# Kernel tuning notes

Measured on AMD Instinct MI355X. Metric: run time of the kernel, lower is better.

Reference implementation:

```python
import jax, jax.numpy as jnp
import numpy as np

L = 2000          # number of residues (sequence length)
FEATURES_L = 2048 # config.features_L pad target
W = 7             # config.window_size
D = 54            # per-residue feature dim after bert_lin
H = 3             # attention heads
HD = D // H       # head dim = 18
CH = 32           # conv hidden channels
KS = (3, 5, 7)    # config.kernels


def setup_inputs() -> dict:
    key = jax.random.key(0)
    ks = jax.random.split(key, 20)
    n = lambda k, s, sc=0.02: jax.random.normal(k, s, jnp.float32) * sc
    return {
        'beft_f': jax.random.normal(ks[0], (L, 1024), jnp.float32),
        'pssm_f': jax.random.normal(ks[1], (L, 20), jnp.float32),
        'hmm_f': jax.random.normal(ks[2], (L, 30), jnp.float32),
        'dssp_f': jax.random.normal(ks[3], (L, 14), jnp.float32),
        'W_bert': n(ks[4], (1024, D)), 'b_bert': jnp.zeros((D,), jnp.float32),
        'ln_g1': jnp.ones((D,), jnp.float32), 'ln_b1': jnp.zeros((D,), jnp.float32),
        'ln_g2': jnp.ones((D,), jnp.float32), 'ln_b2': jnp.zeros((D,), jnp.float32),
        'conv1_w': n(ks[5], (CH, 1, 3, 1), 0.1), 'conv1_b': n(ks[6], (CH,), 0.1),
        'prelu_a': jnp.array(0.25, jnp.float32),
        'conv2_w': n(ks[7], (CH, 1, 5, 1), 0.1), 'conv2_b': n(ks[8], (CH,), 0.1),
        'conv3_w': n(ks[9], (CH, 1, 7, 1), 0.1), 'conv3_b': n(ks[10], (CH,), 0.1),
        'W1': n(ks[11], (972, 256)), 'b1': jnp.zeros((256,), jnp.float32),
        'W2': n(ks[12], (CH * 256, 256)), 'b2': jnp.zeros((256,), jnp.float32),
    }


def _ln(x, g, b, eps=1e-5):
    m = x.mean(-1, keepdims=True)
    v = ((x - m) ** 2).mean(-1, keepdims=True)
    return (x - m) * jax.lax.rsqrt(v + eps) * g + b


def _attn(x, g, b):
    # x: (L, W, D); no qkv projections, no 1/sqrt(d) scaling (as in source)
    qh = x.reshape(x.shape[0], W, H, HD)
    s = jnp.einsum('bqhd,bkhd->bhqk', qh, qh)
    p = jax.nn.softmax(s, axis=-1)
    o = jnp.einsum('bhqk,bkhd->bqhd', p, qh).reshape(x.shape[0], W, D)
    return _ln(o, g, b)


def _conv_branch(x, w, bias, k, act):
    pad = (k - 1) // 2
    c = jax.lax.conv_general_dilated(x, w, (1, 1), ((pad, pad), (0, 0)),
                                     dimension_numbers=('NCHW', 'OIHW', 'NCHW'))
    c = act(c + bias[None, :, None, None])
    c = jax.lax.reduce_window(c, -jnp.inf, jax.lax.max,
                              (1, 1, k, 1), (1, 1, 1, 1), 'VALID')
    return c.reshape(c.shape[0], CH, -1)  # (FEATURES_L, 32, (W-k+1)*2D)


def _forward(beft_f, W_bert, b_bert, ln_g1, ln_b1, ln_g2, ln_b2,
             conv1_w, conv1_b, prelu_a, conv2_w, conv2_b, conv3_w, conv3_b,
             W1, b1, W2, b2):
    f = beft_f @ W_bert + b_bert  # (L, 54)
    # sliding-window gather replicating the source python loop exactly:
    # interior rows i in (W, L-W): window = f[i-4 : i+3]; boundary rows: [f[i], 0...0]
    i = jnp.arange(L)
    j = jnp.arange(W)
    gidx = jnp.clip(i[:, None] - (W // 2 + 1) + j[None, :], 0, L - 1)
    win_int = f[gidx]                                   # (L, 7, 54)
    win_bnd = jnp.zeros((L, W, D), f.dtype).at[:, 0].set(f)
    boundary = (i <= W) | (i + W >= L)
    new_f = jnp.where(boundary[:, None, None], win_bnd, win_int)
    sf = _attn(new_f, ln_g1, ln_b1)
    sf = _attn(sf, ln_g2, ln_b2)
    cat = jnp.concatenate([new_f, sf], axis=2)          # (L, 7, 108)
    x = jnp.pad(cat, ((0, FEATURES_L - L), (0, 0), (0, 0)))[:, None]  # (FL,1,7,108)
    prelu = lambda z: jnp.where(z >= 0, z, prelu_a * z)
    feats = jnp.concatenate([
        _conv_branch(x, conv1_w, conv1_b, KS[0], prelu),
        _conv_branch(x, conv2_w, conv2_b, KS[1], jax.nn.relu),
        _conv_branch(x, conv3_w, conv3_b, KS[2], jax.nn.relu)], axis=2)  # (FL,32,972)
    y = feats[:L] @ W1 + b1                             # (L, 32, 256)
    y = y.reshape(L, CH * 256) @ W2 + b2                # (L, 256)
    return jnp.where(y >= 0, y, 0.01 * y)               # leaky_relu


def reference(beft_f, pssm_f, hmm_f, dssp_f, W_bert, b_bert, ln_g1, ln_b1,
              ln_g2, ln_b2, conv1_w, conv1_b, prelu_a, conv2_w, conv2_b,
              conv3_w, conv3_b, W1, b1, W2, b2):
    # pssm_f / hmm_f / dssp_f are accepted but unused in the source forward
    return _forward(beft_f, W_bert, b_bert, ln_g1, ln_b1, ln_g2, ln_b2,
                    conv1_w, conv1_b, prelu_a, conv2_w, conv2_b,
                    conv3_w, conv3_b, W1, b1, W2, b2)
```

## Files before the change

kernel.cpp:

```cpp
#include <hip/hip_runtime.h>

#define L_RES 2000
#define DF 54
#define WIN 7

typedef short bf16x8 __attribute__((ext_vector_type(8)));
typedef float f32x4 __attribute__((ext_vector_type(4)));
typedef unsigned short ushort8v __attribute__((ext_vector_type(8)));

__device__ __forceinline__ unsigned short f2bf(float f) {
    unsigned int u = __float_as_uint(f);
    unsigned int r = (u + 0x7FFFu + ((u >> 16) & 1u)) >> 16;
    return (unsigned short)r;
}
__device__ __forceinline__ float bf2f(unsigned short h) {
    return __uint_as_float(((unsigned int)h) << 16);
}
__device__ __forceinline__ void gload16(const unsigned short* g, unsigned short* l) {
    __builtin_amdgcn_global_load_lds(
        (const __attribute__((address_space(1))) void*)g,
        (__attribute__((address_space(3))) void*)l, 16, 0, 0);
}

__global__ __launch_bounds__(256) void split_beft(const float* __restrict__ beft,
                                                  unsigned short* __restrict__ A2) {
    int l = blockIdx.x;
    int t = threadIdx.x;
    unsigned short* row = A2 + (size_t)l * 3072;
    for (int k = t; k < 1024; k += 256) {
        unsigned short hi = 0, lo = 0;
        if (l < L_RES) {
            float x = beft[(size_t)l * 1024 + k];
            hi = f2bf(x);
            lo = f2bf(x - bf2f(hi));
        }
        row[k] = hi;
        row[1024 + k] = lo;
        row[2048 + k] = hi;
    }
}

__global__ __launch_bounds__(256) void b2t_build(const float* __restrict__ Wb,
                                                 unsigned short* __restrict__ B2T) {
    int idx = blockIdx.x * 256 + threadIdx.x;
    int n = idx / 3072, col = idx % 3072;
    int seg = col >> 10, k = col & 1023;
    unsigned short r = 0;
    if (n < DF) {
        float v = Wb[(size_t)k * DF + n];
        unsigned short hi = f2bf(v);
        r = (seg < 2) ? hi : f2bf(v - bf2f(hi));
    }
    B2T[idx] = r;
}

__global__ __launch_bounds__(256) void bert_mfma(const unsigned short* __restrict__ A2,
                                                 const unsigned short* __restrict__ B2T,
                                                 float* __restrict__ bpart) {
    __shared__ unsigned short ldsA[128 * 64];
    __shared__ unsigned short ldsB[64 * 64];
    int t = threadIdx.x, w = t >> 6, lane = t & 63;
    int m0 = blockIdx.x * 128;
    int z = blockIdx.y;
    long koff = (long)z * 768;
    int wr = w >> 1, wc = w & 1;
    int arow = lane & 15, kgrp = lane >> 4;

    const unsigned short* aS[4]; const unsigned short* bS[2];
    int aD[4], bD[2];
    #pragma unroll
    for (int j = 0; j < 4; ++j) {
        int s = j * 256 + t, r = s >> 3, c = s & 7;
        aS[j] = A2 + koff + (size_t)(m0 + r) * 3072 + c * 8;
        aD[j] = r * 64 + ((c ^ (r & 7)) * 8);
    }
    #pragma unroll
    for (int j = 0; j < 2; ++j) {
        int s = j * 256 + t, r = s >> 3, c = s & 7;
        bS[j] = B2T + koff + (size_t)r * 3072 + c * 8;
        bD[j] = r * 64 + ((c ^ (r & 7)) * 8);
    }
    f32x4 acc[4][2];
    #pragma unroll
    for (int mi = 0; mi < 4; ++mi)
        #pragma unroll
        for (int ni = 0; ni < 2; ++ni) acc[mi][ni] = (f32x4)(0.f);

    ushort8v va[4], vb[2];
    #pragma unroll
    for (int j = 0; j < 4; ++j) va[j] = *(const ushort8v*)(aS[j]);
    #pragma unroll
    for (int j = 0; j < 2; ++j) vb[j] = *(const ushort8v*)(bS[j]);

    for (int ks = 0; ks < 12; ++ks) {
        __syncthreads();
        #pragma unroll
        for (int j = 0; j < 4; ++j) *(ushort8v*)&ldsA[aD[j]] = va[j];
        #pragma unroll
        for (int j = 0; j < 2; ++j) *(ushort8v*)&ldsB[bD[j]] = vb[j];
        __syncthreads();
        if (ks + 1 < 12) {
            #pragma unroll
            for (int j = 0; j < 4; ++j) va[j] = *(const ushort8v*)(aS[j] + (ks + 1) * 64);
            #pragma unroll
            for (int j = 0; j < 2; ++j) vb[j] = *(const ushort8v*)(bS[j] + (ks + 1) * 64);
        }
        #pragma unroll
        for (int kk = 0; kk < 2; ++kk) {
            int chunk = kk * 4 + kgrp;
            bf16x8 af[4], bfr[2];
            #pragma unroll
            for (int mi = 0; mi < 4; ++mi) {
                int rl = wr * 64 + mi * 16 + arow;
                af[mi] = *(const bf16x8*)&ldsA[rl * 64 + ((chunk ^ (rl & 7)) * 8)];
            }
            #pragma unroll
            for (int ni = 0; ni < 2; ++ni) {
                int rl = wc * 32 + ni * 16 + arow;
                bfr[ni] = *(const bf16x8*)&ldsB[rl * 64 + ((chunk ^ (rl & 7)) * 8)];
            }
            #pragma unroll
            for (int mi = 0; mi < 4; ++mi)
                #pragma unroll
                for (int ni = 0; ni < 2; ++ni)
                    acc[mi][ni] = __builtin_amdgcn_mfma_f32_16x16x32_bf16(af[mi], bfr[ni], acc[mi][ni], 0, 0, 0);
        }
    }
    #pragma unroll
    for (int ni = 0; ni < 2; ++ni) {
        int n = wc * 32 + ni * 16 + arow;
        #pragma unroll
        for (int mi = 0; mi < 4; ++mi)
            #pragma unroll
            for (int r = 0; r < 4; ++r) {
                int m = m0 + wr * 64 + mi * 16 + kgrp * 4 + r;
                bpart[((size_t)z * 2048 + m) * 64 + n] = acc[mi][ni][r];
            }
    }
}

__global__ __launch_bounds__(64) void bert_reduce(const float* __restrict__ bpart,
                                                  const float* __restrict__ bb,
                                                  float* __restrict__ f) {
    int l = blockIdx.x, n = threadIdx.x;
    if (n < DF) {
        float s = bb[n];
        #pragma unroll
        for (int z = 0; z < 4; ++z) s += bpart[((size_t)z * 2048 + l) * 64 + n];
        f[(size_t)l * DF + n] = s;
    }
}

__device__ __forceinline__ void attn_layer_w(const float (*in)[DF], float (*out)[DF],
                                             float (*s)[WIN][WIN],
                                             const float* __restrict__ g,
                                             const float* __restrict__ b,
                                             float* mm, float* vv, int lane) {
    for (int idx = lane; idx < 3 * WIN * WIN; idx += 64) {
        int h = idx / 49, r = idx % 49, q = r / WIN, k = r % WIN;
        float sum = 0.f;
        #pragma unroll
        for (int d = 0; d < 18; ++d) sum = fmaf(in[q][h * 18 + d], in[k][h * 18 + d], sum);
        s[h][q][k] = sum;
    }
    __syncthreads();
    for (int idx = lane; idx < 3 * WIN; idx += 64) {
        int h = idx / WIN, q = idx % WIN;
        float mx = s[h][q][0];
        #pragma unroll
        for (int k = 1; k < WIN; ++k) mx = fmaxf(mx, s[h][q][k]);
        float e[WIN], sum = 0.f;
        #pragma unroll
        for (int k = 0; k < WIN; ++k) { e[k] = expf(s[h][q][k] - mx); sum += e[k]; }
        float inv = 1.f / sum;
        #pragma unroll
        for (int k = 0; k < WIN; ++k) s[h][q][k] = e[k] * inv;
    }
    __syncthreads();
    for (int idx = lane; idx < WIN * DF; idx += 64) {
        int q = idx / DF, c = idx % DF, h = c / 18;
        float sum = 0.f;
        #pragma unroll
        for (int k = 0; k < WIN; ++k) sum = fmaf(s[h][q][k], in[k][c], sum);
        out[q][c] = sum;
    }
    __syncthreads();
    for (int q = lane; q < WIN; q += 64) {
        float m = 0.f;
        for (int c = 0; c < DF; ++c) m += out[q][c];
        m *= (1.f / DF);
        float v = 0.f;
        for (int c = 0; c < DF; ++c) { float d0 = out[q][c] - m; v = fmaf(d0, d0, v); }
        v *= (1.f / DF);
        mm[q] = m; vv[q] = rsqrtf(v + 1e-5f);
    }
    __syncthreads();
    for (int idx = lane; idx < WIN * DF; idx += 64) {
        int q = idx / DF, c = idx % DF;
        out[q][c] = (out[q][c] - mm[q]) * vv[q] * g[c] + b[c];
    }
    __syncthreads();
}

__global__ __launch_bounds__(256) void window_attn4(const float* __restrict__ f,
                                                    const float* __restrict__ g1,
                                                    const float* __restrict__ b1,
                                                    const float* __restrict__ g2,
                                                    const float* __restrict__ b2,
                                                    float* __restrict__ cat) {
    int wv = threadIdx.x >> 6, lane = threadIdx.x & 63;
    int l = blockIdx.x * 4 + wv;
    __shared__ float w[4][WIN][DF], o1[4][WIN][DF], o2[4][WIN][DF];
    __shared__ float s[4][3][WIN][WIN];
    __shared__ float mm[4][WIN], vvv[4][WIN];
    bool boundary = (l <= WIN) || (l + WIN >= L_RES);
    for (int idx = lane; idx < WIN * DF; idx += 64) {
        int j = idx / DF, d = idx % DF;
        w[wv][j][d] = boundary ? (j == 0 ? f[(size_t)l * DF + d] : 0.f)
                               : f[(size_t)(l - 4 + j) * DF + d];
    }
    __syncthreads();
    attn_layer_w(w[wv], o1[wv], s[wv], g1, b1, mm[wv], vvv[wv], lane);
    attn_layer_w(o1[wv], o2[wv], s[wv], g2, b2, mm[wv], vvv[wv], lane);
    for (int idx = lane; idx < WIN * DF; idx += 64) {
        int j = idx / DF, d = idx % DF;
        cat[(size_t)l * 756 + j * 108 + d] = w[wv][j][d];
        cat[(size_t)l * 756 + j * 108 + DF + d] = o2[wv][j][d];
    }
}

__global__ __launch_bounds__(256) void transpose_to_bf16(const float* __restrict__ src,
                                                         unsigned short* __restrict__ dst,
                                                         int M, int N, int Mpad) {
    __shared__ float tile[32][33];
    int m0 = blockIdx.x * 32, n0 = blockIdx.y * 32;
    int c = threadIdx.x % 32, r0 = threadIdx.x / 32;
    #pragma unroll
    for (int rr = 0; rr < 4; ++rr) {
        int r = r0 + rr * 8, m = m0 + r;
        tile[r][c] = (m < M) ? src[(size_t)m * N + n0 + c] : 0.f;
    }
    __syncthreads();
    #pragma unroll
    for (int rr = 0; rr < 4; ++rr) {
        int r = r0 + rr * 8;
        dst[(size_t)(n0 + r) * Mpad + m0 + c] = f2bf(tile[c][r]);
    }
}

__global__ __launch_bounds__(256) void conv_pool(
        const float* __restrict__ cat,
        const float* __restrict__ c1w, const float* __restrict__ c1b,
        const float* __restrict__ pa_p,
        const float* __restrict__ c2w, const float* __restrict__ c2b,
        const float* __restrict__ c3w, const float* __restrict__ c3b,
        unsigned short* __restrict__ Ap, int lbase) {
    int bid = blockIdx.x;
    int b = bid >> 1;
    int ch0 = (bid & 1) * 16;
    int l0 = lbase + b * 4;
    int t = threadIdx.x;
    __shared__ float catl[4 * 756];
    for (int i = t; i < 3024; i += 256) catl[i] = cat[(size_t)l0 * 756 + i];
    __syncthreads();
    float pa = pa_p[0];
    unsigned short* base = Ap + (size_t)b * 128 * 1024;
    int res = t >> 6, dp = t & 63;
    if (dp < 54) {
        int d0 = dp * 2;
        const float* cr = catl + res * 756;
        float colA[WIN], colB[WIN];
        #pragma unroll
        for (int h = 0; h < WIN; ++h) {
            colA[h] = cr[h * 108 + d0];
            colB[h] = cr[h * 108 + d0 + 1];
        }
        for (int c = ch0; c < ch0 + 16; ++c) {
            unsigned short* Arow = base + (size_t)(res * 32 + c) * 1024;
            {
                float w0 = c1w[c * 3], w1 = c1w[c * 3 + 1], w2 = c1w[c * 3 + 2];
                float bb = c1b[c];
                float vA[WIN], vB[WIN];
                #pragma unroll
                for (int h = 0; h < WIN; ++h) {
                    float sA = bb, sB = bb;
                    if (h >= 1) { sA = fmaf(w0, colA[h - 1], sA); sB = fmaf(w0, colB[h - 1], sB); }
                    sA = fmaf(w1, colA[h], sA); sB = fmaf(w1, colB[h], sB);
                    if (h <= 5) { sA = fmaf(w2, colA[h + 1], sA); sB = fmaf(w2, colB[h + 1], sB); }
                    vA[h] = sA >= 0.f ? sA : pa * sA;
                    vB[h] = sB >= 0.f ? sB : pa * sB;
                }
                #pragma unroll
                for (int p = 0; p < 5; ++p) {
                    unsigned int ua = f2bf(fmaxf(fmaxf(vA[p], vA[p + 1]), vA[p + 2]));
                    unsigned int ub = f2bf(fmaxf(fmaxf(vB[p], vB[p + 1]), vB[p + 2]));
                    *(unsigned int*)&Arow[p * 108 + d0] = ua | (ub << 16);
                }
            }
            {
                float wg[5], bb = c2b[c];
                #pragma unroll
                for (int x = 0; x < 5; ++x) wg[x] = c2w[c * 5 + x];
                float vA[WIN], vB[WIN];
                #pragma unroll
                for (int h = 0; h < WIN; ++h) {
                    float sA = bb, sB = bb;
                    #pragma unroll
                    for (int x = 0; x < 5; ++x) {
                        int hh = h + x - 2;
                        if (hh >= 0 && hh <= 6) {
                            sA = fmaf(wg[x], colA[hh], sA);
                            sB = fmaf(wg[x], colB[hh], sB);
                        }
                    }
                    vA[h] = fmaxf(sA, 0.f);
                    vB[h] = fmaxf(sB, 0.f);
                }
                #pragma unroll
                for (int p = 0; p < 3; ++p) {
                    float ma = vA[p], mb = vB[p];
                    #pragma unroll
                    for (int r = 1; r < 5; ++r) { ma = fmaxf(ma, vA[p + r]); mb = fmaxf(mb, vB[p + r]); }
                    unsigned int ua = f2bf(ma), ub = f2bf(mb);
                    *(unsigned int*)&Arow[540 + p * 108 + d0] = ua | (ub << 16);
                }
            }
            {
                float wg[7], bb = c3b[c];
                #pragma unroll
                for (int x = 0; x < 7; ++x) wg[x] = c3w[c * 7 + x];
                float ma = 0.f, mb = 0.f;
                #pragma unroll
                for (int h = 0; h < WIN; ++h) {
                    float sA = bb, sB = bb;
                    #pragma unroll
                    for (int x = 0; x < 7; ++x) {
                        int hh = h + x - 3;
                        if (hh >= 0 && hh <= 6) {
                            sA = fmaf(wg[x], colA[hh], sA);
                            sB = fmaf(wg[x], colB[hh], sB);
                        }
                    }
                    ma = fmaxf(ma, sA);
                    mb = fmaxf(mb, sB);
                }
                unsigned int ua = f2bf(fmaxf(ma, 0.f)), ub = f2bf(fmaxf(mb, 0.f));
                *(unsigned int*)&Arow[864 + d0] = ua | (ub << 16);
            }
        }
    }
    for (int i = t; i < 1664; i += 256) {
        int r = i / 26, q = i - r * 26;
        int res2 = r >> 4, c2 = ch0 + (r & 15);
        *(unsigned int*)&base[(size_t)(res2 * 32 + c2) * 1024 + 972 + q * 2] = 0u;
    }
}

template<bool EPI_BF16, int ZBITS>
__global__ __launch_bounds__(512) void gemm_tile8(
        const unsigned short* __restrict__ A, long lda,
        const unsigned short* __restrict__ B, long ldb,
        int nk, const float* __restrict__ bias,
        unsigned short* __restrict__ outB, float* __restrict__ outF,
        long outRowBase) {
    __shared__ unsigned short ldsA[128 * 64];
    __shared__ unsigned short ldsB[256 * 64];
    int t = threadIdx.x, w = t >> 6, lane = t & 63;
    int bid = blockIdx.x;
    int z = bid & ((1 << ZBITS) - 1);
    long m0 = (long)(bid >> ZBITS) * 128;
    long koff = (long)z * (long)nk * 64;
    A += koff; B += koff;
    int wr = w >> 2, wc = w & 3;
    int arow = lane & 15, kgrp = lane >> 4;
    int ra = lane >> 3, cc = lane & 7;
    int csw = (cc ^ ra) * 8;

    const unsigned short* gA[2]; const unsigned short* gB[4];
    unsigned short* dA[2]; unsigned short* dB[4];
    #pragma unroll
    for (int j = 0; j < 2; ++j) {
        int rbase = j * 64 + w * 8;
        gA[j] = A + (size_t)(m0 + rbase + ra) * lda + csw;
        dA[j] = &ldsA[rbase * 64];
    }
    #pragma unroll
    for (int j = 0; j < 4; ++j) {
        int rbase = j * 64 + w * 8;
        gB[j] = B + (size_t)(rbase + ra) * ldb + csw;
        dB[j] = &ldsB[rbase * 64];
    }
    f32x4 acc[4][4];
    #pragma unroll
    for (int mi = 0; mi < 4; ++mi)
        #pragma unroll
        for (int ni = 0; ni < 4; ++ni) acc[mi][ni] = (f32x4)(0.f);

    for (int ks = 0; ks < nk; ++ks) {
        #pragma unroll
        for (int j = 0; j < 2; ++j) gload16(gA[j] + ks * 64, dA[j]);
        #pragma unroll
        for (int j = 0; j < 4; ++j) gload16(gB[j] + ks * 64, dB[j]);
        __syncthreads();
        #pragma unroll
        for (int kk = 0; kk < 2; ++kk) {
            int chunk = kk * 4 + kgrp;
            bf16x8 af[4], bfr[4];
            #pragma unroll
            for (int mi = 0; mi < 4; ++mi) {
                int rl = wr * 64 + mi * 16 + arow;
                af[mi] = *(const bf16x8*)&ldsA[rl * 64 + ((chunk ^ (rl & 7)) * 8)];
            }
            #pragma unroll
            for (int ni = 0; ni < 4; ++ni) {
                int rl = wc * 64 + ni * 16 + arow;
                bfr[ni] = *(const bf16x8*)&ldsB[rl * 64 + ((chunk ^ (rl & 7)) * 8)];
            }
            #pragma unroll
            for (int mi = 0; mi < 4; ++mi)
                #pragma unroll
                for (int ni = 0; ni < 4; ++ni)
                    acc[mi][ni] = __builtin_amdgcn_mfma_f32_16x16x32_bf16(af[mi], bfr[ni], acc[mi][ni], 0, 0, 0);
        }
        __syncthreads();
    }
    #pragma unroll
    for (int ni = 0; ni < 4; ++ni) {
        int n = wc * 64 + ni * 16 + arow;
        float bv = EPI_BF16 ? bias[n] : 0.f;
        #pragma unroll
        for (int mi = 0; mi < 4; ++mi)
            #pragma unroll
            for (int r = 0; r < 4; ++r) {
                long m = m0 + wr * 64 + mi * 16 + kgrp * 4 + r;
                if (EPI_BF16)
                    outB[(outRowBase + m) * 256 + n] = f2bf(acc[mi][ni][r] + bv);
                else
                    outF[((long)z * 2048 + m) * 256 + n] = acc[mi][ni][r];
            }
    }
}

__global__ __launch_bounds__(256) void reduce2(const float* __restrict__ part,
                                               const float* __restrict__ b2v,
                                               float* __restrict__ out) {
    int l = blockIdx.x, n = threadIdx.x;
    float sum = b2v[n];
    #pragma unroll
    for (int s = 0; s < 8; ++s) sum += part[((size_t)s * 2048 + l) * 256 + n];
    out[(size_t)l * 256 + n] = sum >= 0.f ? sum : 0.01f * sum;
}

extern "C" void kernel_launch(void* const* d_in, const int* in_sizes, int n_in,
                              void* d_out, int out_size, void* d_ws, size_t ws_size,
                              hipStream_t stream) {
    const float* beft = (const float*)d_in[0];
    const float* Wb  = (const float*)d_in[4];
    const float* bb  = (const float*)d_in[5];
    const float* g1  = (const float*)d_in[6];
    const float* b1  = (const float*)d_in[7];
    const float* g2  = (const float*)d_in[8];
    const float* b2  = (const float*)d_in[9];
    const float* c1w = (const float*)d_in[10];
    const float* c1b = (const float*)d_in[11];
    const float* pa  = (const float*)d_in[12];
    const float* c2w = (const float*)d_in[13];
    const float* c2b = (const float*)d_in[14];
    const float* c3w = (const float*)d_in[15];
    const float* c3b = (const float*)d_in[16];
    const float* W1  = (const float*)d_in[17];
    const float* b1v = (const float*)d_in[18];
    const float* W2  = (const float*)d_in[19];
    const float* b2v = (const float*)d_in[20];
    float* out = (float*)d_out;
    char* ws = (char*)d_ws;

    float*          f    = (float*)(ws + 0);
    float*          cat  = (float*)(ws + 524288);
    unsigned short* W1T  = (unsigned short*)(ws + 8388608);
    unsigned short* W2T  = (unsigned short*)(ws + 8912896);
    unsigned short* y1   = (unsigned short*)(ws + 13107200);
    unsigned short* A2   = (unsigned short*)(ws + 13107200);
    unsigned short* B2T  = (unsigned short*)(ws + 25690112);
    float*          bpart= (float*)(ws + 46661632);
    unsigned short* Ap   = (unsigned short*)(ws + 46661632);
    float*          part = (float*)(ws + 46661632);

    long avail = (long)ws_size - 46661632L;
    long tpc = avail / (128L * 1024L * 2L);
    if (tpc < 1) tpc = 1;
    if (tpc > 500) tpc = 500;

    split_beft<<<2048, 256, 0, stream>>>(beft, A2);
    b2t_build<<<768, 256, 0, stream>>>(Wb, B2T);
    bert_mfma<<<dim3(16, 4), 256, 0, stream>>>(A2, B2T, bpart);
    bert_reduce<<<L_RES, 64, 0, stream>>>(bpart, bb, f);
    window_attn4<<<500, 256, 0, stream>>>(f, g1, b1, g2, b2, cat);
    transpose_to_bf16<<<dim3(32, 8), 256, 0, stream>>>(W1, W1T, 972, 256, 1024);
    transpose_to_bf16<<<dim3(256, 8), 256, 0, stream>>>(W2, W2T, 8192, 256, 8192);

    for (long t0 = 0; t0 < 500; t0 += tpc) {
        long nt = (500 - t0 < tpc) ? (500 - t0) : tpc;
        conv_pool<<<(int)(nt * 2), 256, 0, stream>>>(cat, c1w, c1b, pa, c2w, c2b,
                                                     c3w, c3b, Ap, (int)(t0 * 4));
        gemm_tile8<true, 0><<<(int)nt, 512, 0, stream>>>(
            Ap, 1024, W1T, 1024, 16, b1v, y1, nullptr, t0 * 128);
    }
    gemm_tile8<false, 3><<<128, 512, 0, stream>>>(
        y1, 8192, W2T, 8192, 16, nullptr, nullptr, part, 0);
    reduce2<<<L_RES, 256, 0, stream>>>(part, b2v, out);
}
```

Before: 155.3 us.

## Fuse conv/pool feature build with first GEMM in shared memory

Replaces the conv_pool kernel plus separate gemm_tile8 launch with a single kernel that builds the pooled conv features for 4 residues in a 128KB LDS buffer and runs the W1 MFMA GEMM directly from LDS in two K-halves of 512. This removes the global-memory round trip of the 128x1024 bf16 feature matrix and the chunked launch loop. In exchange, the whole 128KB LDS allocation limits occupancy to one block per CU, the conv work is recomputed partially across halves, and W1T fragments are read straight from global without staging.

New measurement: 186.1 us. 19.9% more time.

```diff
diff --git a/kernel.cpp b/kernel.cpp
--- a/kernel.cpp
+++ b/kernel.cpp
@@ -248,54 +248,117 @@
     }
 }
 
-__global__ __launch_bounds__(256) void conv_pool(
+__global__ __launch_bounds__(512) void conv_gemm1f(
         const float* __restrict__ cat,
         const float* __restrict__ c1w, const float* __restrict__ c1b,
         const float* __restrict__ pa_p,
         const float* __restrict__ c2w, const float* __restrict__ c2b,
         const float* __restrict__ c3w, const float* __restrict__ c3b,
-        unsigned short* __restrict__ Ap, int lbase) {
-    int bid = blockIdx.x;
-    int b = bid >> 1;
-    int ch0 = (bid & 1) * 16;
-    int l0 = lbase + b * 4;
+        const unsigned short* __restrict__ W1T, const float* __restrict__ b1v,
+        unsigned short* __restrict__ y1) {
+    __shared__ unsigned short Abuf[128 * 512];
     int t = threadIdx.x;
-    __shared__ float catl[4 * 756];
-    for (int i = t; i < 3024; i += 256) catl[i] = cat[(size_t)l0 * 756 + i];
-    __syncthreads();
+    int l0 = blockIdx.x * 4;
+    int w = t >> 6, lane = t & 63;
+    int wr = w >> 2, wc = w & 3;
+    int arow = lane & 15, kgrp = lane >> 4;
+
+    int res = t >> 7, half = (t >> 6) & 1, dp = lane;
+    bool act = dp < 54;
+    int d0 = dp * 2;
     float pa = pa_p[0];
-    unsigned short* base = Ap + (size_t)b * 128 * 1024;
-    int res = t >> 6, dp = t & 63;
-    if (dp < 54) {
-        int d0 = dp * 2;
-        const float* cr = catl + res * 756;
-        float colA[WIN], colB[WIN];
+    float colA[WIN], colB[WIN];
+    if (act) {
+        const float* cr = cat + (size_t)(l0 + res) * 756;
         #pragma unroll
         for (int h = 0; h < WIN; ++h) {
             colA[h] = cr[h * 108 + d0];
             colB[h] = cr[h * 108 + d0 + 1];
         }
-        for (int c = ch0; c < ch0 + 16; ++c) {
-            unsigned short* Arow = base + (size_t)(res * 32 + c) * 1024;
-            {
+    }
+    f32x4 acc[4][4];
+    #pragma unroll
+    for (int mi = 0; mi < 4; ++mi)
+        #pragma unroll
+        for (int ni = 0; ni < 4; ++ni) acc[mi][ni] = (f32x4)(0.f);
+
+    if (act) {
+        for (int c = half * 16; c < half * 16 + 16; ++c) {
+            int row = res * 32 + c;
+            float w0 = c1w[c * 3], w1 = c1w[c * 3 + 1], w2 = c1w[c * 3 + 2];
+            float bb = c1b[c];
+            float vA[WIN], vB[WIN];
+            #pragma unroll
+            for (int h = 0; h < WIN; ++h) {
+                float sA = bb, sB = bb;
+                if (h >= 1) { sA = fmaf(w0, colA[h - 1], sA); sB = fmaf(w0, colB[h - 1], sB); }
+                sA = fmaf(w1, colA[h], sA); sB = fmaf(w1, colB[h], sB);
+                if (h <= 5) { sA = fmaf(w2, colA[h + 1], sA); sB = fmaf(w2, colB[h + 1], sB); }
+                vA[h] = sA >= 0.f ? sA : pa * sA;
+                vB[h] = sB >= 0.f ? sB : pa * sB;
+            }
+            #pragma unroll
+            for (int p = 0; p < 5; ++p) {
+                int col = p * 108 + d0;
+                if (col < 512) {
+                    unsigned int ua = f2bf(fmaxf(fmaxf(vA[p], vA[p + 1]), vA[p + 2]));
+                    unsigned int ub = f2bf(fmaxf(fmaxf(vB[p], vB[p + 1]), vB[p + 2]));
+                    *(unsigned int*)&Abuf[row * 512 + (col ^ ((row & 7) << 3))] = ua | (ub << 16);
+                }
+            }
+        }
+    }
+    __syncthreads();
+    #pragma unroll 1
+    for (int ks = 0; ks < 8; ++ks) {
+        #pragma unroll
+        for (int kk = 0; kk < 2; ++kk) {
+            int G = ks * 8 + kk * 4 + kgrp;
+            bf16x8 af[4], bfr[4];
+            #pragma unroll
+            for (int ni = 0; ni < 4; ++ni) {
+                int n = wc * 64 + ni * 16 + arow;
+                bfr[ni] = *(const bf16x8*)&W1T[(size_t)n * 1024 + G * 8];
+            }
+            #pragma unroll
+            for (int mi = 0; mi < 4; ++mi) {
+                int rl = wr * 64 + mi * 16 + arow;
+                af[mi] = *(const bf16x8*)&Abuf[rl * 512 + ((G ^ (rl & 7)) << 3)];
+            }
+            #pragma unroll
+            for (int mi = 0; mi < 4; ++mi)
+                #pragma unroll
+                for (int ni = 0; ni < 4; ++ni)
+                    acc[mi][ni] = __builtin_amdgcn_mfma_f32_16x16x32_bf16(af[mi], bfr[ni], acc[mi][ni], 0, 0, 0);
+        }
+    }
+    __syncthreads();
+    for (int i = t; i < 128 * 26; i += 512) {
+        int row = i / 26, q = i - (i / 26) * 26;
+        int col = 460 + q * 2;
+        *(unsigned int*)&Abuf[row * 512 + (col ^ ((row & 7) << 3))] = 0u;
+    }
+    if (act) {
+        for (int c = half * 16; c < half * 16 + 16; ++c) {
+            int row = res * 32 + c;
+            if (d0 >= 80) {
                 float w0 = c1w[c * 3], w1 = c1w[c * 3 + 1], w2 = c1w[c * 3 + 2];
                 float bb = c1b[c];
-                float vA[WIN], vB[WIN];
-                #pragma unroll
-                for (int h = 0; h < WIN; ++h) {
+                float vA[3], vB[3];
+                #pragma unroll
+                for (int j = 0; j < 3; ++j) {
+                    int h = 4 + j;
                     float sA = bb, sB = bb;
-                    if (h >= 1) { sA = fmaf(w0, colA[h - 1], sA); sB = fmaf(w0, colB[h - 1], sB); }
-                    sA = fmaf(w1, colA[h], sA); sB = fmaf(w1, colB[h], sB);
+                    sA = fmaf(w0, colA[h - 1], sA); sB = fmaf(w0, colB[h - 1], sB);
+                    sA = fmaf(w1, colA[h], sA);     sB = fmaf(w1, colB[h], sB);
                     if (h <= 5) { sA = fmaf(w2, colA[h + 1], sA); sB = fmaf(w2, colB[h + 1], sB); }
-                    vA[h] = sA >= 0.f ? sA : pa * sA;
-                    vB[h] = sB >= 0.f ? sB : pa * sB;
+                    vA[j] = sA >= 0.f ? sA : pa * sA;
+                    vB[j] = sB >= 0.f ? sB : pa * sB;
                 }
-                #pragma unroll
-                for (int p = 0; p < 5; ++p) {
-                    unsigned int ua = f2bf(fmaxf(fmaxf(vA[p], vA[p + 1]), vA[p + 2]));
-                    unsigned int ub = f2bf(fmaxf(fmaxf(vB[p], vB[p + 1]), vB[p + 2]));
-                    *(unsigned int*)&Arow[p * 108 + d0] = ua | (ub << 16);
-                }
+                unsigned int ua = f2bf(fmaxf(fmaxf(vA[0], vA[1]), vA[2]));
+                unsigned int ub = f2bf(fmaxf(fmaxf(vB[0], vB[1]), vB[2]));
+                int col = d0 - 80;
+                *(unsigned int*)&Abuf[row * 512 + (col ^ ((row & 7) << 3))] = ua | (ub << 16);
             }
             {
                 float wg[5], bb = c2b[c];
@@ -322,7 +385,8 @@
                     #pragma unroll
                     for (int r = 1; r < 5; ++r) { ma = fmaxf(ma, vA[p + r]); mb = fmaxf(mb, vB[p + r]); }
                     unsigned int ua = f2bf(ma), ub = f2bf(mb);
-                    *(unsigned int*)&Arow[540 + p * 108 + d0] = ua | (ub << 16);
+                    int col = 28 + p * 108 + d0;
+                    *(unsigned int*)&Abuf[row * 512 + (col ^ ((row & 7) << 3))] = ua | (ub << 16);
                 }
             }
             {
@@ -345,14 +409,54 @@
                     mb = fmaxf(mb, sB);
                 }
                 unsigned int ua = f2bf(fmaxf(ma, 0.f)), ub = f2bf(fmaxf(mb, 0.f));
-                *(unsigned int*)&Arow[864 + d0] = ua | (ub << 16);
-            }
-        }
-    }
-    for (int i = t; i < 1664; i += 256) {
-        int r = i / 26, q = i - r * 26;
-        int res2 = r >> 4, c2 = ch0 + (r & 15);
-        *(unsigned int*)&base[(size_t)(res2 * 32 + c2) * 1024 + 972 + q * 2] = 0u;
+                int col = 352 + d0;
+                *(unsigned int*)&Abuf[row * 512 + (col ^ ((row & 7) << 3))] = ua | (ub << 16);
+            }
+        }
+    }
+    __syncthreads();
+    #pragma unroll 1
+    for (int ks = 0; ks < 8; ++ks) {
+        #pragma unroll
+        for (int kk = 0; kk < 2; ++kk) {
+            int G = ks * 8 + kk * 4 + kgrp;
+            bf16x8 af[4], bfr[4];
+            #pragma unroll
+            for (int ni = 0; ni < 4; ++ni) {
+                int n = wc * 64 + ni * 16 + arow;
+                bfr[ni] = *(const bf16x8*)&W1T[(size_t)n * 1024 + 512 + G * 8];
+            }
+            #pragma unroll
+            for (int mi = 0; mi < 4; ++mi) {
+                int rl = wr * 64 + mi * 16 + arow;
+                af[mi] = *(const bf16x8*)&Abuf[rl * 512 + ((G ^ (rl & 7)) << 3)];
+            }
+            #pragma unroll
+            for (int mi = 0; mi < 4; ++mi)
+                #pragma unroll
+                for (int ni = 0; ni < 4; ++ni)
+                    acc[mi][ni] = __builtin_amdgcn_mfma_f32_16x16x32_bf16(af[mi], bfr[ni], acc[mi][ni], 0, 0, 0);
+        }
+    }
+    __syncthreads();
+    #pragma unroll
+    for (int ni = 0; ni < 4; ++ni) {
+        int n = wc * 64 + ni * 16 + arow;
+        float bv = b1v[n];
+        #pragma unroll
+        for (int mi = 0; mi < 4; ++mi)
+            #pragma unroll
+            for (int r = 0; r < 4; ++r) {
+                int row = wr * 64 + mi * 16 + kgrp * 4 + r;
+                Abuf[row * 256 + n] = f2bf(acc[mi][ni][r] + bv);
+            }
+    }
+    __syncthreads();
+    unsigned short* dst = y1 + (size_t)blockIdx.x * 32768;
+    #pragma unroll
+    for (int i = 0; i < 8; ++i) {
+        int e = (i * 512 + t) * 8;
+        *(ushort8v*)&dst[e] = *(const ushort8v*)&Abuf[e];
     }
 }
 
@@ -483,13 +587,7 @@
     unsigned short* A2   = (unsigned short*)(ws + 13107200);
     unsigned short* B2T  = (unsigned short*)(ws + 25690112);
     float*          bpart= (float*)(ws + 46661632);
-    unsigned short* Ap   = (unsigned short*)(ws + 46661632);
     float*          part = (float*)(ws + 46661632);
-
-    long avail = (long)ws_size - 46661632L;
-    long tpc = avail / (128L * 1024L * 2L);
-    if (tpc < 1) tpc = 1;
-    if (tpc > 500) tpc = 500;
 
     split_beft<<<2048, 256, 0, stream>>>(beft, A2);
     b2t_build<<<768, 256, 0, stream>>>(Wb, B2T);
@@ -499,13 +597,8 @@
     transpose_to_bf16<<<dim3(32, 8), 256, 0, stream>>>(W1, W1T, 972, 256, 1024);
     transpose_to_bf16<<<dim3(256, 8), 256, 0, stream>>>(W2, W2T, 8192, 256, 8192);
 
-    for (long t0 = 0; t0 < 500; t0 += tpc) {
-        long nt = (500 - t0 < tpc) ? (500 - t0) : tpc;
-        conv_pool<<<(int)(nt * 2), 256, 0, stream>>>(cat, c1w, c1b, pa, c2w, c2b,
-                                                     c3w, c3b, Ap, (int)(t0 * 4));
-        gemm_tile8<true, 0><<<(int)nt, 512, 0, stream>>>(
-            Ap, 1024, W1T, 1024, 16, b1v, y1, nullptr, t0 * 128);
-    }
+    conv_gemm1f<<<500, 512, 0, stream>>>(cat, c1w, c1b, pa, c2w, c2b, c3w, c3b,
+                                         W1T, b1v, y1);
     gemm_tile8<false, 3><<<128, 512, 0, stream>>>(
         y1, 8192, W2T, 8192, 16, nullptr, nullptr, part, 0);
     reduce2<<<L_RES, 256, 0, stream>>>(part, b2v, out);
```
